# Optimization experiments

Measured on AMD Instinct MI355X. Metric: run time of the kernel, lower is better.

The kernel has to match this reference:

```python
import jax, jax.numpy as jnp
import numpy as np
from jax import lax

L, H, DH, D, FF = 8, 16, 64, 1024, 4096  # layers, heads, head dim, model dim, mlp hidden
B, S = 4, 512
EPS = 1e-5


def setup_inputs() -> dict:
    key = jax.random.key(0)
    ks = jax.random.split(key, 8)
    std = 0.02
    return {
        "x": jax.random.normal(ks[0], (B, S, D), jnp.float32),
        "ln1_w": jnp.ones((L, D), jnp.float32),
        "ln1_b": jnp.zeros((L, D), jnp.float32),
        "qw": jax.random.normal(ks[1], (L, H, DH, DH), jnp.float32) * std,
        "qb": jnp.zeros((L, H, DH), jnp.float32),
        "kw": jax.random.normal(ks[2], (L, H, DH, DH), jnp.float32) * std,
        "kb": jnp.zeros((L, H, DH), jnp.float32),
        "vw": jax.random.normal(ks[3], (L, H, DH, DH), jnp.float32) * std,
        "vb": jnp.zeros((L, H, DH), jnp.float32),
        "ln2_w": jnp.ones((L, D), jnp.float32),
        "ln2_b": jnp.zeros((L, D), jnp.float32),
        "w1": jax.random.normal(ks[4], (L, D, FF), jnp.float32) * std,
        "b1": jnp.zeros((L, FF), jnp.float32),
        "w2": jax.random.normal(ks[5], (L, FF, D), jnp.float32) * std,
        "b2": jnp.zeros((L, D), jnp.float32),
    }


def _layernorm(x, w, b):
    m = jnp.mean(x, axis=-1, keepdims=True)
    v = jnp.mean(jnp.square(x - m), axis=-1, keepdims=True)
    return (x - m) * lax.rsqrt(v + EPS) * w + b


def reference(x, ln1_w, ln1_b, qw, qb, kw, kb, vw, vb, ln2_w, ln2_b, w1, b1, w2, b2):
    b, s, d = x.shape
    scale = 1.0 / jnp.sqrt(jnp.asarray(DH, x.dtype))

    def layer(h, p):
        (l1w, l1b, Qw, Qb, Kw, Kb, Vw, Vb, l2w, l2b, W1, B1, W2, B2) = p
        y = _layernorm(h, l1w, l1b)
        yh = y.reshape(b, s, H, DH)
        # nn.Linear per head: y @ W.T + b, W is [out=e, in=d]
        q = jnp.einsum('bshd,hed->bshe', yh, Qw) + Qb
        k = jnp.einsum('bshd,hed->bshe', yh, Kw) + Kb
        v = jnp.einsum('bshd,hed->bshe', yh, Vw) + Vb
        attn = jax.nn.softmax(jnp.einsum('bshe,bthe->bhst', q, k) * scale, axis=-1)
        o = jnp.einsum('bhst,bthe->bshe', attn, v).reshape(b, s, d)
        h = h + o
        z = _layernorm(h, l2w, l2b)
        z = jax.nn.gelu(z @ W1 + B1, approximate=False) @ W2 + B2
        return h + z, None

    params = (ln1_w, ln1_b, qw, qb, kw, kb, vw, vb, ln2_w, ln2_b, w1, b1, w2, b2)
    out, _ = lax.scan(layer, x, params)
    return out
```

## Files before the change

### kernel.cpp

```cpp
#include <hip/hip_runtime.h>
#include <hip/hip_bf16.h>

typedef __hip_bfloat16 bf16;
typedef __bf16 bf16x8 __attribute__((ext_vector_type(8)));
typedef float f32x4 __attribute__((ext_vector_type(4)));
typedef unsigned short u16;
typedef unsigned int u32;

#define SEQ 512
#define DMODEL 1024
#define FFDIM 4096
#define NHEAD 16
#define HDIM 64
#define NB 4
#define NLAYER 8

__device__ __forceinline__ u16 f2bu(float f) {
    union { bf16 h; u16 u; } c; c.h = __float2bfloat16(f); return c.u;
}

__device__ __forceinline__ void gload16(const bf16* g, bf16* l) {
    __builtin_amdgcn_global_load_lds(
        (const __attribute__((address_space(1))) unsigned int*)g,
        (__attribute__((address_space(3))) unsigned int*)l,
        16, 0, 0);
}

template<int BM, int BN, int BK, int WM, int WN>
__device__ __forceinline__ void gemm_core(
    const bf16* __restrict__ A, int lda,
    const bf16* __restrict__ B, int ldb,
    int K,
    f32x4 (&acc)[WM/16][WN/16],
    bf16* lA, bf16* lB)
{
    constexpr int NFM = WM / 16, NFN = WN / 16;
    constexpr int WC = BN / WN;
    const int tid  = threadIdx.x;
    const int lane = tid & 63, wave = tid >> 6;
    const int wr = wave / WC, wc = wave % WC;
    const int l15 = lane & 15, l4 = lane >> 4;

    constexpr int ITA = (BM * BK) / (256 * 8);
    constexpr int ITB = (BN * BK) / (256 * 8);

    for (int kt = 0; kt < K; kt += BK) {
        __syncthreads();
#pragma unroll
        for (int it = 0; it < ITA; ++it) {
            const int f = (it * 256 + tid) * 8;
            const int r = f / BK, c = f % BK;
            gload16(A + (long)r * lda + kt + c, lA + f);
        }
#pragma unroll
        for (int it = 0; it < ITB; ++it) {
            const int f = (it * 256 + tid) * 8;
            const int r = f / BK, c = f % BK;
            gload16(B + (long)r * ldb + kt + c, lB + f);
        }
        __syncthreads();
#pragma unroll
        for (int ks = 0; ks < BK / 32; ++ks) {
            bf16x8 af[NFM], bfr[NFN];
#pragma unroll
            for (int fm = 0; fm < NFM; ++fm)
                af[fm] = *(const bf16x8*)(lA + (wr * WM + fm * 16 + l15) * BK + ks * 32 + l4 * 8);
#pragma unroll
            for (int fn = 0; fn < NFN; ++fn)
                bfr[fn] = *(const bf16x8*)(lB + (wc * WN + fn * 16 + l15) * BK + ks * 32 + l4 * 8);
#pragma unroll
            for (int fm = 0; fm < NFM; ++fm)
#pragma unroll
                for (int fn = 0; fn < NFN; ++fn)
                    acc[fm][fn] = __builtin_amdgcn_mfma_f32_16x16x32_bf16(
                        af[fm], bfr[fn], acc[fm][fn], 0, 0, 0);
        }
    }
}

__global__ __launch_bounds__(256) void k_ln(const float* __restrict__ h,
                                            const float* __restrict__ w,
                                            const float* __restrict__ bp,
                                            bf16* __restrict__ out)
{
    const int row = blockIdx.x;
    const int tid = threadIdx.x;
    const float4 x = ((const float4*)(h + (long)row * DMODEL))[tid];
    float s  = x.x + x.y + x.z + x.w;
    float s2 = x.x * x.x + x.y * x.y + x.z * x.z + x.w * x.w;
#pragma unroll
    for (int off = 32; off; off >>= 1) { s += __shfl_xor(s, off); s2 += __shfl_xor(s2, off); }
    __shared__ float rs[4], rs2[4];
    const int wave = tid >> 6;
    if ((tid & 63) == 0) { rs[wave] = s; rs2[wave] = s2; }
    __syncthreads();
    const float S1 = rs[0] + rs[1] + rs[2] + rs[3];
    const float S2 = rs2[0] + rs2[1] + rs2[2] + rs2[3];
    const float mean = S1 * (1.0f / DMODEL);
    const float var  = S2 * (1.0f / DMODEL) - mean * mean;
    const float rstd = rsqrtf(var + 1e-5f);
    const float4 wv = ((const float4*)w)[tid];
    const float4 bv = ((const float4*)bp)[tid];
    uint2 o;
    o.x = (u32)f2bu((x.x - mean) * rstd * wv.x + bv.x) |
          ((u32)f2bu((x.y - mean) * rstd * wv.y + bv.y) << 16);
    o.y = (u32)f2bu((x.z - mean) * rstd * wv.z + bv.z) |
          ((u32)f2bu((x.w - mean) * rstd * wv.w + bv.w) << 16);
    ((uint2*)(out + (long)row * DMODEL))[tid] = o;
}

__global__ __launch_bounds__(256) void k_cvt_qkvw(const float* __restrict__ qw,
                                                  const float* __restrict__ kw,
                                                  const float* __restrict__ vw,
                                                  bf16* __restrict__ wq)
{
    const int i = blockIdx.x * 256 + threadIdx.x;
    const int sel = i >> 14;
    const int off = i & 16383;
    const float* s = (sel == 0) ? qw : (sel == 1) ? kw : vw;
    const float4 v = ((const float4*)s)[off];
    uint2 o;
    o.x = (u32)f2bu(v.x) | ((u32)f2bu(v.y) << 16);
    o.y = (u32)f2bu(v.z) | ((u32)f2bu(v.w) << 16);
    ((uint2*)wq)[i] = o;
}

__global__ __launch_bounds__(256) void k_transw(const float* __restrict__ w1,
                                                const float* __restrict__ w2,
                                                bf16* __restrict__ w1t,
                                                bf16* __restrict__ w2t)
{
    __shared__ float t[64][65];
    int bid = blockIdx.x;
    const float* src; bf16* dst; int R, C, rb, cb;
    if (bid < 1024) {
        src = w1; dst = w1t; R = DMODEL; C = FFDIM;
        rb = (bid >> 6) << 6; cb = (bid & 63) << 6;
    } else {
        bid -= 1024;
        src = w2; dst = w2t; R = FFDIM; C = DMODEL;
        rb = (bid >> 4) << 6; cb = (bid & 15) << 6;
    }
    const int tid = threadIdx.x;
#pragma unroll
    for (int i = 0; i < 16; ++i) {
        int flat = i * 256 + tid;
        int r = flat >> 6, c = flat & 63;
        t[r][c] = src[(long)(rb + r) * C + cb + c];
    }
    __syncthreads();
#pragma unroll
    for (int i = 0; i < 16; ++i) {
        int flat = i * 256 + tid;
        int c = flat >> 6, r = flat & 63;
        dst[(long)(cb + c) * R + rb + r] = __float2bfloat16(t[r][c]);
    }
}

__global__ __launch_bounds__(256) void k_qkv2(const bf16* __restrict__ y,
                                              const bf16* __restrict__ wq,
                                              const float* __restrict__ qb,
                                              const float* __restrict__ kb,
                                              const float* __restrict__ vb,
                                              bf16* __restrict__ qh,
                                              bf16* __restrict__ kh,
                                              bf16* __restrict__ vt)
{
    __shared__ __align__(16) char lmem[128 * 64 * 2 + 64 * 64 * 2];
    bf16* lA = (bf16*)lmem;
    char* lBb = lmem + 128 * 64 * 2;

    const int tid = threadIdx.x;
    const int lane = tid & 63, wave = tid >> 6;
    const int l15 = lane & 15, l4 = lane >> 4;
    const int z = blockIdx.y;
    const int b = z >> 4, hd = z & 15;
    const bf16* A = y + (long)b * SEQ * DMODEL + hd * HDIM + (long)blockIdx.x * 128 * DMODEL;

#pragma unroll
    for (int it = 0; it < 4; ++it) {
        const int f = (it * 256 + tid) * 8;
        const int r = f >> 6, c = f & 63;
        gload16(A + (long)r * DMODEL + c, lA + f);
    }
    __syncthreads();

    bf16x8 qa[2][2];
#pragma unroll
    for (int fm = 0; fm < 2; ++fm)
#pragma unroll
        for (int ks = 0; ks < 2; ++ks)
            qa[fm][ks] = *(const bf16x8*)(lA + (wave * 32 + fm * 16 + l15) * 64 + ks * 32 + l4 * 8);

    for (int t = 0; t < 3; ++t) {
        __syncthreads();
        const bf16* Bsrc = wq + (long)(t * NHEAD + hd) * HDIM * HDIM;
#pragma unroll
        for (int it = 0; it < 2; ++it) {
            const int f = (it * 256 + tid) * 8;
            const int r = f >> 6;
            const uint4 v = *(const uint4*)(Bsrc + f);
            int byte = (f << 1) ^ ((r & 7) << 4);
            *(uint4*)(lBb + byte) = v;
        }
        __syncthreads();

        bf16x8 bfr[4][2];
#pragma unroll
        for (int fn = 0; fn < 4; ++fn)
#pragma unroll
            for (int ks = 0; ks < 2; ++ks) {
                const int row = fn * 16 + l15;
                int byte = (row << 7) + ((ks * 32 + l4 * 8) << 1);
                byte ^= (row & 7) << 4;
                bfr[fn][ks] = *(const bf16x8*)(lBb + byte);
            }
        f32x4 acc[2][4] = {};
#pragma unroll
        for (int ks = 0; ks < 2; ++ks)
#pragma unroll
            for (int fm = 0; fm < 2; ++fm)
#pragma unroll
                for (int fn = 0; fn < 4; ++fn)
                    acc[fm][fn] = __builtin_amdgcn_mfma_f32_16x16x32_bf16(
                        qa[fm][ks], bfr[fn][ks], acc[fm][fn], 0, 0, 0);

        const float* bias = (t == 0) ? qb : (t == 1) ? kb : vb;
#pragma unroll
        for (int fm = 0; fm < 2; ++fm)
#pragma unroll
            for (int fn = 0; fn < 4; ++fn)
#pragma unroll
                for (int r = 0; r < 4; ++r) {
                    const int srow = blockIdx.x * 128 + wave * 32 + fm * 16 + l4 * 4 + r;
                    const int e = fn * 16 + l15;
                    float v = acc[fm][fn][r] + bias[hd * HDIM + e];
                    if (t == 0) {
                        qh[((long)z * SEQ + srow) * HDIM + e] = __float2bfloat16(v * 0.125f);
                    } else if (t == 1) {
                        kh[((long)z * SEQ + srow) * HDIM + e] = __float2bfloat16(v);
                    } else {
                        vt[((long)z * HDIM + e) * SEQ + srow] = __float2bfloat16(v);
                    }
                }
    }
}

__global__ __launch_bounds__(256) void k_flash(const bf16* __restrict__ qh,
                                               const bf16* __restrict__ kh,
                                               const bf16* __restrict__ vt,
                                               float* __restrict__ h)
{
    __shared__ __align__(16) char lmem[24576];
    bf16* lQ = (bf16*)lmem;
    char* lKb = lmem + 8192;
    char* lVb = lmem + 16384;

    const int tid = threadIdx.x;
    const int lane = tid & 63, wave = tid >> 6;
    const int l15 = lane & 15, l4 = lane >> 4;
    const int z = blockIdx.y;
    const int b = z >> 4, hd = z & 15;
    const int q0 = blockIdx.x * 64;

    const bf16* Qsrc = qh + ((long)z * SEQ + q0) * HDIM;
#pragma unroll
    for (int it = 0; it < 2; ++it) {
        const int f = (it * 256 + tid) * 8;
        gload16(Qsrc + f, lQ + f);
    }
    __syncthreads();

    bf16x8 qa[2];
#pragma unroll
    for (int ks = 0; ks < 2; ++ks)
        qa[ks] = *(const bf16x8*)(lQ + (wave * 16 + l15) * 64 + ks * 32 + l4 * 8);

    char* lPb = lmem + wave * 2048;

    f32x4 O[4] = {};
    float mrun[4], lrun[4];
#pragma unroll
    for (int r = 0; r < 4; ++r) { mrun[r] = -1e30f; lrun[r] = 0.0f; }

    for (int kv = 0; kv < SEQ / 64; ++kv) {
        __syncthreads();
        const bf16* Ksrc = kh + ((long)z * SEQ + kv * 64) * HDIM;
#pragma unroll
        for (int it = 0; it < 2; ++it) {
            const int f = (it * 256 + tid) * 8;
            const int r = f >> 6;
            const uint4 v = *(const uint4*)(Ksrc + f);
            *(uint4*)(lKb + ((f << 1) ^ ((r & 7) << 4))) = v;
        }
        const bf16* Vsrc = vt + (long)z * HDIM * SEQ + kv * 64;
#pragma unroll
        for (int it = 0; it < 2; ++it) {
            const int f = (it * 256 + tid) * 8;
            const int r = f >> 6, c = f & 63;
            const uint4 v = *(const uint4*)(Vsrc + (long)r * SEQ + c);
            *(uint4*)(lVb + ((f << 1) ^ ((r & 7) << 4))) = v;
        }
        __syncthreads();

        f32x4 sa[4];
#pragma unroll
        for (int fn = 0; fn < 4; ++fn) sa[fn] = (f32x4){0.f, 0.f, 0.f, 0.f};
#pragma unroll
        for (int ks = 0; ks < 2; ++ks)
#pragma unroll
            for (int fn = 0; fn < 4; ++fn) {
                const int row = fn * 16 + l15;
                int byte = (row << 7) + ((ks * 32 + l4 * 8) << 1);
                byte ^= (row & 7) << 4;
                const bf16x8 kb_ = *(const bf16x8*)(lKb + byte);
                sa[fn] = __builtin_amdgcn_mfma_f32_16x16x32_bf16(qa[ks], kb_, sa[fn], 0, 0, 0);
            }

#pragma unroll
        for (int r = 0; r < 4; ++r) {
            float mx = fmaxf(fmaxf(sa[0][r], sa[1][r]), fmaxf(sa[2][r], sa[3][r]));
#pragma unroll
            for (int m_ = 1; m_ < 16; m_ <<= 1) mx = fmaxf(mx, __shfl_xor(mx, m_));
            const float nm = fmaxf(mrun[r], mx);
            const float al = __expf(mrun[r] - nm);
            mrun[r] = nm;
            float p0 = __expf(sa[0][r] - nm), p1 = __expf(sa[1][r] - nm);
            float p2 = __expf(sa[2][r] - nm), p3 = __expf(sa[3][r] - nm);
            float ps = p0 + p1 + p2 + p3;
#pragma unroll
            for (int m_ = 1; m_ < 16; m_ <<= 1) ps += __shfl_xor(ps, m_);
            lrun[r] = lrun[r] * al + ps;
#pragma unroll
            for (int fn = 0; fn < 4; ++fn) O[fn][r] *= al;
            const int row = l4 * 4 + r;
            const int rsw = (row & 7) << 4;
            const int rb = row << 7;
            *(u16*)(lPb + ((rb + ((0 * 16 + l15) << 1)) ^ rsw)) = f2bu(p0);
            *(u16*)(lPb + ((rb + ((1 * 16 + l15) << 1)) ^ rsw)) = f2bu(p1);
            *(u16*)(lPb + ((rb + ((2 * 16 + l15) << 1)) ^ rsw)) = f2bu(p2);
            *(u16*)(lPb + ((rb + ((3 * 16 + l15) << 1)) ^ rsw)) = f2bu(p3);
        }

#pragma unroll
        for (int ks = 0; ks < 2; ++ks) {
            const int rowp = l15;
            int pbyte = (rowp << 7) + ((ks * 32 + l4 * 8) << 1);
            pbyte ^= (rowp & 7) << 4;
            const bf16x8 pa = *(const bf16x8*)(lPb + pbyte);
#pragma unroll
            for (int fn = 0; fn < 4; ++fn) {
                const int row = fn * 16 + l15;
                int byte = (row << 7) + ((ks * 32 + l4 * 8) << 1);
                byte ^= (row & 7) << 4;
                const bf16x8 vb_ = *(const bf16x8*)(lVb + byte);
                O[fn] = __builtin_amdgcn_mfma_f32_16x16x32_bf16(pa, vb_, O[fn], 0, 0, 0);
            }
        }
    }

    float rinv[4];
#pragma unroll
    for (int r = 0; r < 4; ++r) rinv[r] = 1.0f / lrun[r];
#pragma unroll
    for (int fn = 0; fn < 4; ++fn)
#pragma unroll
        for (int r = 0; r < 4; ++r) {
            const int srow = q0 + wave * 16 + l4 * 4 + r;
            const int e = fn * 16 + l15;
            h[((long)b * SEQ + srow) * DMODEL + hd * HDIM + e] += O[fn][r] * rinv[r];
        }
}

__global__ __launch_bounds__(256) void k_gemm1(const bf16* __restrict__ zb,
                                               const bf16* __restrict__ w1t,
                                               const float* __restrict__ b1,
                                               bf16* __restrict__ ff1)
{
    constexpr int BM = 64, BN = 128, BK = 64, WM = 32, WN = 64;
    __shared__ __align__(16) bf16 lA[BM * BK];
    __shared__ __align__(16) bf16 lB[BN * BK];
    const bf16* A = zb + (long)blockIdx.x * BM * DMODEL;
    const bf16* B = w1t + (long)blockIdx.y * BN * DMODEL;
    f32x4 acc[2][4] = {};
    gemm_core<BM, BN, BK, WM, WN>(A, DMODEL, B, DMODEL, DMODEL, acc, lA, lB);

    const int lane = threadIdx.x & 63, wave = threadIdx.x >> 6;
    const int wr = wave >> 1, wc = wave & 1, l15 = lane & 15, l4 = lane >> 4;
#pragma unroll
    for (int fm = 0; fm < 2; ++fm)
#pragma unroll
        for (int fn = 0; fn < 4; ++fn)
#pragma unroll
            for (int r = 0; r < 4; ++r) {
                const int row = blockIdx.x * BM + wr * WM + fm * 16 + l4 * 4 + r;
                const int col = blockIdx.y * BN + wc * WN + fn * 16 + l15;
                const float x = acc[fm][fn][r] + b1[col];
                const float g = 0.5f * x * (1.0f + erff(x * 0.70710678118f));
                ff1[(long)row * FFDIM + col] = __float2bfloat16(g);
            }
}

__global__ __launch_bounds__(256) void k_gemm2(const bf16* __restrict__ ff1,
                                               const bf16* __restrict__ w2t,
                                               float* __restrict__ part)
{
    constexpr int BM = 64, BN = 128, BK = 64, WM = 32, WN = 64;
    constexpr int KSPLIT = FFDIM / 4;
    __shared__ __align__(16) bf16 lA[BM * BK];
    __shared__ __align__(16) bf16 lB[BN * BK];
    const int sk = blockIdx.z;
    const bf16* A = ff1 + (long)blockIdx.x * BM * FFDIM + (long)sk * KSPLIT;
    const bf16* B = w2t + (long)blockIdx.y * BN * FFDIM + (long)sk * KSPLIT;
    f32x4 acc[2][4] = {};
    gemm_core<BM, BN, BK, WM, WN>(A, FFDIM, B, FFDIM, KSPLIT, acc, lA, lB);

    float* out = part + (long)sk * (NB * SEQ) * DMODEL;
    const int lane = threadIdx.x & 63, wave = threadIdx.x >> 6;
    const int wr = wave >> 1, wc = wave & 1, l15 = lane & 15, l4 = lane >> 4;
#pragma unroll
    for (int fm = 0; fm < 2; ++fm)
#pragma unroll
        for (int fn = 0; fn < 4; ++fn)
#pragma unroll
            for (int r = 0; r < 4; ++r) {
                const int row = blockIdx.x * BM + wr * WM + fm * 16 + l4 * 4 + r;
                const int col = blockIdx.y * BN + wc * WN + fn * 16 + l15;
                out[(long)row * DMODEL + col] = acc[fm][fn][r];
            }
}

__global__ __launch_bounds__(256) void k_red2ln(const float* __restrict__ part,
                                                const float* __restrict__ b2,
                                                float* __restrict__ h,
                                                const float* __restrict__ lnw,
                                                const float* __restrict__ lnb,
                                                bf16* __restrict__ y,
                                                int do_ln)
{
    constexpr long NELT = (long)NB * SEQ * DMODEL / 4;
    const long row = blockIdx.x;
    const int tid = threadIdx.x;
    const long i = row * (DMODEL / 4) + tid;
    float4 s = ((const float4*)part)[i];
    const float4 s1 = ((const float4*)part)[i + NELT];
    const float4 s2 = ((const float4*)part)[i + 2 * NELT];
    const float4 s3 = ((const float4*)part)[i + 3 * NELT];
    const float4 bv = ((const float4*)b2)[tid];
    float4 hv = ((float4*)h)[i];
    hv.x += s.x + s1.x + s2.x + s3.x + bv.x;
    hv.y += s.y + s1.y + s2.y + s3.y + bv.y;
    hv.z += s.z + s1.z + s2.z + s3.z + bv.z;
    hv.w += s.w + s1.w + s2.w + s3.w + bv.w;
    ((float4*)h)[i] = hv;

    if (!do_ln) return;
    float ss  = hv.x + hv.y + hv.z + hv.w;
    float ss2 = hv.x * hv.x + hv.y * hv.y + hv.z * hv.z + hv.w * hv.w;
#pragma unroll
    for (int off = 32; off; off >>= 1) { ss += __shfl_xor(ss, off); ss2 += __shfl_xor(ss2, off); }
    __shared__ float rs[4], rs2[4];
    const int wave = tid >> 6;
    if ((tid & 63) == 0) { rs[wave] = ss; rs2[wave] = ss2; }
    __syncthreads();
    const float S1 = rs[0] + rs[1] + rs[2] + rs[3];
    const float S2 = rs2[0] + rs2[1] + rs2[2] + rs2[3];
    const float mean = S1 * (1.0f / DMODEL);
    const float var  = S2 * (1.0f / DMODEL) - mean * mean;
    const float rstd = rsqrtf(var + 1e-5f);
    const float4 wv = ((const float4*)lnw)[tid];
    const float4 lb = ((const float4*)lnb)[tid];
    uint2 o;
    o.x = (u32)f2bu((hv.x - mean) * rstd * wv.x + lb.x) |
          ((u32)f2bu((hv.y - mean) * rstd * wv.y + lb.y) << 16);
    o.y = (u32)f2bu((hv.z - mean) * rstd * wv.z + lb.z) |
          ((u32)f2bu((hv.w - mean) * rstd * wv.w + lb.w) << 16);
    ((uint2*)(y + row * DMODEL))[tid] = o;
}

extern "C" void kernel_launch(void* const* d_in, const int* in_sizes, int n_in,
                              void* d_out, int out_size, void* d_ws, size_t ws_size,
                              hipStream_t stream)
{
    const float* x    = (const float*)d_in[0];
    const float* ln1w = (const float*)d_in[1];
    const float* ln1b = (const float*)d_in[2];
    const float* qw   = (const float*)d_in[3];
    const float* qb   = (const float*)d_in[4];
    const float* kw   = (const float*)d_in[5];
    const float* kb   = (const float*)d_in[6];
    const float* vw   = (const float*)d_in[7];
    const float* vb   = (const float*)d_in[8];
    const float* ln2w = (const float*)d_in[9];
    const float* ln2b = (const float*)d_in[10];
    const float* w1   = (const float*)d_in[11];
    const float* b1   = (const float*)d_in[12];
    const float* w2   = (const float*)d_in[13];
    const float* b2   = (const float*)d_in[14];

    char* ws = (char*)d_ws;
    const size_t MB = 1024 * 1024;
    bf16* y    = (bf16*)(ws + 0 * MB);
    bf16* zb   = (bf16*)(ws + 4 * MB);
    bf16* qh   = (bf16*)(ws + 8 * MB);
    bf16* kh   = (bf16*)(ws + 12 * MB);
    bf16* vt   = (bf16*)(ws + 16 * MB);
    bf16* ff1  = (bf16*)(ws + 20 * MB);
    bf16* w1t  = (bf16*)(ws + 36 * MB);
    bf16* w2t  = (bf16*)(ws + 44 * MB);
    bf16* wqkv = (bf16*)(ws + 52 * MB);
    float* part = (float*)(ws + 53 * MB);

    float* h = (float*)d_out;
    hipMemcpyAsync(d_out, x, (size_t)NB * SEQ * DMODEL * sizeof(float),
                   hipMemcpyDeviceToDevice, stream);

    k_ln<<<NB * SEQ, 256, 0, stream>>>(h, ln1w, ln1b, y);

    for (int l = 0; l < NLAYER; ++l) {
        k_cvt_qkvw<<<192, 256, 0, stream>>>(qw + (long)l * 65536, kw + (long)l * 65536,
                                            vw + (long)l * 65536, wqkv);
        k_qkv2<<<dim3(4, NB * NHEAD), 256, 0, stream>>>(
            y, wqkv, qb + l * NHEAD * HDIM, kb + l * NHEAD * HDIM, vb + l * NHEAD * HDIM,
            qh, kh, vt);
        k_flash<<<dim3(SEQ / 64, NB * NHEAD), 256, 0, stream>>>(qh, kh, vt, h);
        k_ln<<<NB * SEQ, 256, 0, stream>>>(h, ln2w + l * DMODEL, ln2b + l * DMODEL, zb);
        k_transw<<<2048, 256, 0, stream>>>(w1 + (long)l * DMODEL * FFDIM,
                                           w2 + (long)l * DMODEL * FFDIM, w1t, w2t);
        k_gemm1<<<dim3(32, 32), 256, 0, stream>>>(zb, w1t, b1 + l * FFDIM, ff1);
        k_gemm2<<<dim3(32, 8, 4), 256, 0, stream>>>(ff1, w2t, part);
        const int last = (l == NLAYER - 1);
        k_red2ln<<<NB * SEQ, 256, 0, stream>>>(part, b2 + l * DMODEL, h,
                                               ln1w + (l + 1) * DMODEL * (1 - last),
                                               ln1b + (l + 1) * DMODEL * (1 - last),
                                               y, !last);
    }
}
```

Measured before the change: 1.127 ms.

## Fuse QKV weight conversion into projection kernel and enlarge FFN GEMM tiles

Drops the separate per-layer kernel that converted QKV weights to bf16. The projection kernel now reads fp32 weights directly and converts them while staging into shared memory, saving one launch and one round trip through memory per layer. Separately, both FFN GEMMs move from 64x128 to 128x128 block tiles with 64x64 per-wave tiles, which raises data reuse but halves the grid and doubles accumulator registers, so occupancy may drop. The gemm2 grid becomes 512 blocks, which may fill the CUs less evenly.

```diff
diff --git a/kernel.cpp b/kernel.cpp
--- a/kernel.cpp
+++ b/kernel.cpp
@@ -109,22 +109,6 @@
     ((uint2*)(out + (long)row * DMODEL))[tid] = o;
 }
 
-__global__ __launch_bounds__(256) void k_cvt_qkvw(const float* __restrict__ qw,
-                                                  const float* __restrict__ kw,
-                                                  const float* __restrict__ vw,
-                                                  bf16* __restrict__ wq)
-{
-    const int i = blockIdx.x * 256 + threadIdx.x;
-    const int sel = i >> 14;
-    const int off = i & 16383;
-    const float* s = (sel == 0) ? qw : (sel == 1) ? kw : vw;
-    const float4 v = ((const float4*)s)[off];
-    uint2 o;
-    o.x = (u32)f2bu(v.x) | ((u32)f2bu(v.y) << 16);
-    o.y = (u32)f2bu(v.z) | ((u32)f2bu(v.w) << 16);
-    ((uint2*)wq)[i] = o;
-}
-
 __global__ __launch_bounds__(256) void k_transw(const float* __restrict__ w1,
                                                 const float* __restrict__ w2,
                                                 bf16* __restrict__ w1t,
@@ -158,7 +142,9 @@
 }
 
 __global__ __launch_bounds__(256) void k_qkv2(const bf16* __restrict__ y,
-                                              const bf16* __restrict__ wq,
+                                              const float* __restrict__ qwl,
+                                              const float* __restrict__ kwl,
+                                              const float* __restrict__ vwl,
                                               const float* __restrict__ qb,
                                               const float* __restrict__ kb,
                                               const float* __restrict__ vb,
@@ -194,14 +180,17 @@
 
     for (int t = 0; t < 3; ++t) {
         __syncthreads();
-        const bf16* Bsrc = wq + (long)(t * NHEAD + hd) * HDIM * HDIM;
-#pragma unroll
-        for (int it = 0; it < 2; ++it) {
-            const int f = (it * 256 + tid) * 8;
-            const int r = f >> 6;
-            const uint4 v = *(const uint4*)(Bsrc + f);
-            int byte = (f << 1) ^ ((r & 7) << 4);
-            *(uint4*)(lBb + byte) = v;
+        const float* Bsrc = ((t == 0) ? qwl : (t == 1) ? kwl : vwl) + (long)hd * HDIM * HDIM;
+#pragma unroll
+        for (int it = 0; it < 4; ++it) {
+            const int f = (it * 256 + tid) * 4;
+            const float4 v = *(const float4*)(Bsrc + f);
+            uint2 o;
+            o.x = (u32)f2bu(v.x) | ((u32)f2bu(v.y) << 16);
+            o.y = (u32)f2bu(v.z) | ((u32)f2bu(v.w) << 16);
+            const int row = f >> 6;
+            const int byte = (f << 1) ^ ((row & 7) << 4);
+            *(uint2*)(lBb + byte) = o;
         }
         __syncthreads();
 
@@ -377,18 +366,18 @@
                                                const float* __restrict__ b1,
                                                bf16* __restrict__ ff1)
 {
-    constexpr int BM = 64, BN = 128, BK = 64, WM = 32, WN = 64;
+    constexpr int BM = 128, BN = 128, BK = 64, WM = 64, WN = 64;
     __shared__ __align__(16) bf16 lA[BM * BK];
     __shared__ __align__(16) bf16 lB[BN * BK];
     const bf16* A = zb + (long)blockIdx.x * BM * DMODEL;
     const bf16* B = w1t + (long)blockIdx.y * BN * DMODEL;
-    f32x4 acc[2][4] = {};
+    f32x4 acc[4][4] = {};
     gemm_core<BM, BN, BK, WM, WN>(A, DMODEL, B, DMODEL, DMODEL, acc, lA, lB);
 
     const int lane = threadIdx.x & 63, wave = threadIdx.x >> 6;
     const int wr = wave >> 1, wc = wave & 1, l15 = lane & 15, l4 = lane >> 4;
 #pragma unroll
-    for (int fm = 0; fm < 2; ++fm)
+    for (int fm = 0; fm < 4; ++fm)
 #pragma unroll
         for (int fn = 0; fn < 4; ++fn)
 #pragma unroll
@@ -405,21 +394,21 @@
                                                const bf16* __restrict__ w2t,
                                                float* __restrict__ part)
 {
-    constexpr int BM = 64, BN = 128, BK = 64, WM = 32, WN = 64;
+    constexpr int BM = 128, BN = 128, BK = 64, WM = 64, WN = 64;
     constexpr int KSPLIT = FFDIM / 4;
     __shared__ __align__(16) bf16 lA[BM * BK];
     __shared__ __align__(16) bf16 lB[BN * BK];
     const int sk = blockIdx.z;
     const bf16* A = ff1 + (long)blockIdx.x * BM * FFDIM + (long)sk * KSPLIT;
     const bf16* B = w2t + (long)blockIdx.y * BN * FFDIM + (long)sk * KSPLIT;
-    f32x4 acc[2][4] = {};
+    f32x4 acc[4][4] = {};
     gemm_core<BM, BN, BK, WM, WN>(A, FFDIM, B, FFDIM, KSPLIT, acc, lA, lB);
 
     float* out = part + (long)sk * (NB * SEQ) * DMODEL;
     const int lane = threadIdx.x & 63, wave = threadIdx.x >> 6;
     const int wr = wave >> 1, wc = wave & 1, l15 = lane & 15, l4 = lane >> 4;
 #pragma unroll
-    for (int fm = 0; fm < 2; ++fm)
+    for (int fm = 0; fm < 4; ++fm)
 #pragma unroll
         for (int fn = 0; fn < 4; ++fn)
 #pragma unroll
@@ -508,7 +497,6 @@
     bf16* ff1  = (bf16*)(ws + 20 * MB);
     bf16* w1t  = (bf16*)(ws + 36 * MB);
     bf16* w2t  = (bf16*)(ws + 44 * MB);
-    bf16* wqkv = (bf16*)(ws + 52 * MB);
     float* part = (float*)(ws + 53 * MB);
 
     float* h = (float*)d_out;
@@ -518,17 +506,16 @@
     k_ln<<<NB * SEQ, 256, 0, stream>>>(h, ln1w, ln1b, y);
 
     for (int l = 0; l < NLAYER; ++l) {
-        k_cvt_qkvw<<<192, 256, 0, stream>>>(qw + (long)l * 65536, kw + (long)l * 65536,
-                                            vw + (long)l * 65536, wqkv);
         k_qkv2<<<dim3(4, NB * NHEAD), 256, 0, stream>>>(
-            y, wqkv, qb + l * NHEAD * HDIM, kb + l * NHEAD * HDIM, vb + l * NHEAD * HDIM,
+            y, qw + (long)l * 65536, kw + (long)l * 65536, vw + (long)l * 65536,
+            qb + l * NHEAD * HDIM, kb + l * NHEAD * HDIM, vb + l * NHEAD * HDIM,
             qh, kh, vt);
         k_flash<<<dim3(SEQ / 64, NB * NHEAD), 256, 0, stream>>>(qh, kh, vt, h);
         k_ln<<<NB * SEQ, 256, 0, stream>>>(h, ln2w + l * DMODEL, ln2b + l * DMODEL, zb);
         k_transw<<<2048, 256, 0, stream>>>(w1 + (long)l * DMODEL * FFDIM,
                                            w2 + (long)l * DMODEL * FFDIM, w1t, w2t);
-        k_gemm1<<<dim3(32, 32), 256, 0, stream>>>(zb, w1t, b1 + l * FFDIM, ff1);
-        k_gemm2<<<dim3(32, 8, 4), 256, 0, stream>>>(ff1, w2t, part);
+        k_gemm1<<<dim3(16, 32), 256, 0, stream>>>(zb, w1t, b1 + l * FFDIM, ff1);
+        k_gemm2<<<dim3(16, 8, 4), 256, 0, stream>>>(ff1, w2t, part);
         const int last = (l == NLAYER - 1);
         k_red2ln<<<NB * SEQ, 256, 0, stream>>>(part, b2 + l * DMODEL, h,
                                                ln1w + (l + 1) * DMODEL * (1 - last),
```

New measurement: 1.008 ms. 10.5% less time.
